# Kernel optimization log

Hardware: AMD Instinct MI355X
Metric: run time of the kernel (lower is better)

## Reference

```python
import jax, jax.numpy as jnp
import numpy as np
import math

B, L, D, P = 2, 2048, 256, 32
PI = math.pi


def _layernorm(x, g, b, eps=1e-5):
    m = x.mean(-1, keepdims=True)
    v = x.var(-1, keepdims=True)
    return (x - m) / jnp.sqrt(v + eps) * g + b


def setup_inputs() -> dict:
    key = jax.random.key(0)
    ks = jax.random.split(key, 16)
    sd = 1.0 / math.sqrt(D)
    f32 = jnp.float32
    inp = {
        "x": jax.random.normal(ks[0], (B, L, D), f32),
        # key_encoder: Linear(D, P)
        "key_W": jax.random.normal(ks[1], (D, P), f32) * sd,
        "key_b": jnp.zeros((P,), f32),
        # value_encoder: Linear(D, D)
        "val_W": jax.random.normal(ks[2], (D, D), f32) * sd,
        "val_b": jnp.zeros((D,), f32),
        # refiner: LayerNorm(D), Linear(D, 2D), GELU, Linear(2D, D)
        "ln1_g": jnp.ones((D,), f32),
        "ln1_b": jnp.zeros((D,), f32),
        "W1": jax.random.normal(ks[3], (D, 2 * D), f32) * sd,
        "b1": jnp.zeros((2 * D,), f32),
        "W2": jax.random.normal(ks[4], (2 * D, D), f32) * (1.0 / math.sqrt(2 * D)),
        "b2": jnp.zeros((D,), f32),
        # to_out: LayerNorm(D), Linear(D, D)
        "ln2_g": jnp.ones((D,), f32),
        "ln2_b": jnp.zeros((D,), f32),
        "Wo": jax.random.normal(ks[5], (D, D), f32) * sd,
        "bo": jnp.zeros((D,), f32),
    }
    return inp


def reference(x, key_W, key_b, val_W, val_b, ln1_g, ln1_b, W1, b1, W2, b2,
              ln2_g, ln2_b, Wo, bo):
    # key phases in (-pi, pi); phasor exp(i*theta) handled as (cos, sin)
    phases = jnp.tanh(x @ key_W + key_b) * PI          # (B, L, P)
    values = x @ val_W + val_b                          # (B, L, D)

    cos_p = jnp.cos(phases)
    sin_p = jnp.sin(phases)
    # torch.roll(shifts=1, dims=1) then zero the first position -> shift right, row 0 = 0
    zrow = jnp.zeros_like(cos_p[:, :1])
    cos_s = jnp.concatenate([zrow, cos_p[:, :-1]], axis=1)
    sin_s = jnp.concatenate([zrow, sin_p[:, :-1]], axis=1)

    # odd positions hold values
    vmask = (jnp.arange(L) % 2 == 1).astype(x.dtype)    # (L,)
    mv = values * vmask[None, :, None]                  # (B, L, D)

    # bind: outer product phasor (P) x value (D); real/imag parts
    bound_re = cos_s[..., None] * mv[:, :, None, :]     # (B, L, P, D)
    bound_im = sin_s[..., None] * mv[:, :, None, :]
    mem_re = jnp.cumsum(bound_re, axis=1)
    mem_im = jnp.cumsum(bound_im, axis=1)

    # retrieve: Re[ memory * exp(-i*theta) ] summed over phases
    retrieved = (jnp.einsum('blpd,blp->bld', mem_re, cos_p)
                 + jnp.einsum('blpd,blp->bld', mem_im, sin_p))

    valid = jnp.maximum(jnp.cumsum(vmask), 1.0)         # (L,)
    retrieved = retrieved / (jnp.sqrt(valid)[None, :, None] * math.sqrt(P))

    h = _layernorm(retrieved, ln1_g, ln1_b)
    h = jax.nn.gelu(h @ W1 + b1, approximate=False)
    refined = h @ W2 + b2
    out = x + (_layernorm(refined, ln2_g, ln2_b) @ Wo + bo)
    return out
```

## Files before the change

### kernel.cpp

```cpp
#include <hip/hip_runtime.h>
#include <math.h>

#define BB 2
#define LL 2048
#define DD 256
#define PP 32
#define NC 64
#define PI_F 3.14159265358979323846f

typedef __attribute__((ext_vector_type(8))) short bf16x8;
typedef __attribute__((ext_vector_type(4))) float f32x4;
typedef unsigned short ushort_t;
typedef unsigned int uint_t;

__device__ inline ushort_t f2bf(float x) {
    uint_t u = __float_as_uint(x);
    uint_t r = (u + 0x7fffu + ((u >> 16) & 1u)) >> 16;
    return (ushort_t)r;
}

__global__ __launch_bounds__(256) void prep_key_kernel(
    const float* __restrict__ W1, const float* __restrict__ W2,
    const float* __restrict__ Wo, const float* __restrict__ valW,
    const float* __restrict__ x, const float* __restrict__ key_W,
    const float* __restrict__ key_b,
    ushort_t* __restrict__ W1t, ushort_t* __restrict__ W2t,
    ushort_t* __restrict__ Wot, ushort_t* __restrict__ valWt,
    float2* __restrict__ ph)
{
    const int bid = blockIdx.x;
    const int t = threadIdx.x;
    if (bid < 96) {
        __shared__ float T[64][65];
        const float* W; ushort_t* Wt; int K, N, tile;
        if (bid < 32)      { W = W1;   Wt = W1t;   K = 256; N = 512; tile = bid; }
        else if (bid < 64) { W = W2;   Wt = W2t;   K = 512; N = 256; tile = bid - 32; }
        else if (bid < 80) { W = Wo;   Wt = Wot;   K = 256; N = 256; tile = bid - 64; }
        else               { W = valW; Wt = valWt; K = 256; N = 256; tile = bid - 80; }
        const int ntiles = N / 64;
        const int k0 = (tile / ntiles) * 64, n0 = (tile % ntiles) * 64;
        {
            const int rr = t >> 2, cb = (t & 3) * 16;
            #pragma unroll
            for (int i = 0; i < 16; i += 4) {
                const float4 v = *(const float4*)&W[(k0 + rr) * N + n0 + cb + i];
                T[rr][cb + i + 0] = v.x; T[rr][cb + i + 1] = v.y;
                T[rr][cb + i + 2] = v.z; T[rr][cb + i + 3] = v.w;
            }
        }
        __syncthreads();
        {
            const int n = t >> 2, kb = (t & 3) * 16;
            #pragma unroll
            for (int i = 0; i < 16; ++i)
                Wt[(n0 + n) * K + k0 + kb + i] = f2bf(T[kb + i][n]);
        }
    } else {
        __shared__ ushort_t xt[16][264];
        __shared__ ushort_t kwT[32][264];
        __shared__ float rbuf[4][2][16][17];
        const int row0 = (bid - 96) * 16;
        {
            const int l = t >> 4, cb = (t & 15) * 16;
            const float* src = &x[(long)(row0 + l) * DD + cb];
            ushort_t tmp[16];
            #pragma unroll
            for (int i = 0; i < 4; ++i) {
                const float4 v = *(const float4*)&src[i * 4];
                tmp[i*4+0] = f2bf(v.x); tmp[i*4+1] = f2bf(v.y);
                tmp[i*4+2] = f2bf(v.z); tmp[i*4+3] = f2bf(v.w);
            }
            *(uint4*)&xt[l][cb]     = *(uint4*)&tmp[0];
            *(uint4*)&xt[l][cb + 8] = *(uint4*)&tmp[8];
        }
        {
            #pragma unroll
            for (int i = 0; i < 8; ++i) {
                const int idx4 = i * 256 + t;
                const int k = idx4 >> 3, pc = (idx4 & 7) * 4;
                const float4 v = *(const float4*)&key_W[k * 32 + pc];
                kwT[pc + 0][k] = f2bf(v.x);
                kwT[pc + 1][k] = f2bf(v.y);
                kwT[pc + 2][k] = f2bf(v.z);
                kwT[pc + 3][k] = f2bf(v.w);
            }
        }
        __syncthreads();
        const int wv = t >> 6, lane = t & 63;
        const int qd = lane >> 4, mc = lane & 15;
        f32x4 acc0 = {0.f,0.f,0.f,0.f}, acc1 = {0.f,0.f,0.f,0.f};
        #pragma unroll
        for (int ks = 0; ks < 2; ++ks) {
            const int ko = wv * 64 + ks * 32 + qd * 8;
            const bf16x8 a  = *(const bf16x8*)&xt[mc][ko];
            const bf16x8 b0 = *(const bf16x8*)&kwT[mc][ko];
            const bf16x8 b1 = *(const bf16x8*)&kwT[16 + mc][ko];
            acc0 = __builtin_amdgcn_mfma_f32_16x16x32_bf16(a, b0, acc0, 0, 0, 0);
            acc1 = __builtin_amdgcn_mfma_f32_16x16x32_bf16(a, b1, acc1, 0, 0, 0);
        }
        #pragma unroll
        for (int r = 0; r < 4; ++r) {
            rbuf[wv][0][qd * 4 + r][mc] = acc0[r];
            rbuf[wv][1][qd * 4 + r][mc] = acc1[r];
        }
        __syncthreads();
        #pragma unroll
        for (int rep = 0; rep < 2; ++rep) {
            const int idx = rep * 256 + t;
            const int p = idx & 31, l = idx >> 5;
            const int nf = p >> 4, mcol = p & 15;
            float a = key_b[p] + rbuf[0][nf][l][mcol] + rbuf[1][nf][l][mcol]
                    + rbuf[2][nf][l][mcol] + rbuf[3][nf][l][mcol];
            a = tanhf(a) * PI_F;
            float sn, cs;
            sincosf(a, &sn, &cs);
            ph[(long)(row0 + l) * PP + p] = make_float2(cs, sn);
        }
    }
}

__global__ __launch_bounds__(256) void valbind_kernel(
    const float* __restrict__ x, const float2* __restrict__ ph,
    const ushort_t* __restrict__ valWt, const float* __restrict__ val_b,
    ushort_t* __restrict__ VoddT, float* __restrict__ Mt)
{
    __shared__ ushort_t xsb[16][264];
    __shared__ ushort_t VdT[64][40];
    __shared__ ushort_t phsT[64][40];
    __shared__ float    Ms[64][68];

    const int tid = threadIdx.x;
    const int bid = blockIdx.x;
    const int b  = bid >> 8;
    const int c  = (bid >> 2) & 63;
    const int dq = bid & 3;
    const int base = b * LL;
    const int r0 = 32 * c;

    {
        const int j = tid >> 4, cb = (tid & 15) * 16;
        const float* src = &x[(long)(base + r0 + 2 * j + 1) * DD + cb];
        ushort_t tmp[16];
        #pragma unroll
        for (int i = 0; i < 4; ++i) {
            const float4 v = *(const float4*)&src[i * 4];
            tmp[i*4+0] = f2bf(v.x); tmp[i*4+1] = f2bf(v.y);
            tmp[i*4+2] = f2bf(v.z); tmp[i*4+3] = f2bf(v.w);
        }
        *(uint4*)&xsb[j][cb]     = *(uint4*)&tmp[0];
        *(uint4*)&xsb[j][cb + 8] = *(uint4*)&tmp[8];
    }
    {
        const int j = tid >> 4, qb = (tid & 15) * 4;
        const float4 v = *(const float4*)((const float*)ph +
                              (long)(base + r0 + 2 * j) * 64 + qb);
        phsT[qb + 0][j] = f2bf(v.x);
        phsT[qb + 1][j] = f2bf(v.y);
        phsT[qb + 2][j] = f2bf(v.z);
        phsT[qb + 3][j] = f2bf(v.w);
    }
    for (int e = tid; e < 64 * 16; e += 256) {
        phsT[e >> 4][16 + (e & 15)] = 0;
        VdT[e >> 4][16 + (e & 15)] = 0;
    }
    __syncthreads();

    const int wv = tid >> 6, lane = tid & 63;
    const int qd = lane >> 4, mc = lane & 15;

    f32x4 va = {0.f,0.f,0.f,0.f};
    const int dloc = wv * 16 + mc;
    const int ng = dq * 64 + dloc;
    const ushort_t* B0 = &valWt[(long)ng * 256];
    #pragma unroll
    for (int ks = 0; ks < 8; ++ks) {
        const bf16x8 a  = *(const bf16x8*)&xsb[mc][ks * 32 + qd * 8];
        const bf16x8 b0 = *(const bf16x8*)&B0[ks * 32 + qd * 8];
        va = __builtin_amdgcn_mfma_f32_16x16x32_bf16(a, b0, va, 0, 0, 0);
    }
    {
        const float bb = val_b[ng];
        #pragma unroll
        for (int r = 0; r < 4; ++r)
            VdT[dloc][qd * 4 + r] = f2bf(va[r] + bb);
    }
    __syncthreads();

    const bf16x8 a2 = *(const bf16x8*)&phsT[wv * 16 + mc][qd * 8];
    f32x4 macc[4];
    #pragma unroll
    for (int nf = 0; nf < 4; ++nf) {
        f32x4 z = {0.f,0.f,0.f,0.f};
        const bf16x8 b2 = *(const bf16x8*)&VdT[nf * 16 + mc][qd * 8];
        macc[nf] = __builtin_amdgcn_mfma_f32_16x16x32_bf16(a2, b2, z, 0, 0, 0);
    }
    #pragma unroll
    for (int nf = 0; nf < 4; ++nf) {
        #pragma unroll
        for (int r = 0; r < 4; ++r)
            Ms[nf * 16 + mc][wv * 16 + qd * 4 + r] = macc[nf][r];
    }
    __syncthreads();

    {
        float* dst = &Mt[((long)(b * NC + c) * 256 + dq * 64) * 64];
        #pragma unroll
        for (int p = 0; p < 4; ++p) {
            const int idx4 = p * 256 + tid;
            const int dl = idx4 >> 4, q4 = (idx4 & 15) * 4;
            *(float4*)&dst[dl * 64 + q4] = *(const float4*)&Ms[dl][q4];
        }
    }
    if (tid < 64) {
        ushort_t* vd = &VoddT[((long)(b * NC + c) * 256 + dq * 64 + tid) * 16];
        *(uint4*)&vd[0] = *(const uint4*)&VdT[tid][0];
        *(uint4*)&vd[8] = *(const uint4*)&VdT[tid][8];
    }
}

__global__ __launch_bounds__(256) void prefix_kernel(
    const float* __restrict__ M, ushort_t* __restrict__ Mpre_b)
{
    __shared__ float segsum[4][64];
    const int tid = threadIdx.x;
    const int b  = blockIdx.x >> 8;
    const int cg = blockIdx.x & 255;
    const int col = cg * 64 + (tid & 63);
    const int seg = tid >> 6;
    const long base = (long)b * NC * 16384 + col;

    float v[16], s = 0.f;
    #pragma unroll
    for (int i = 0; i < 16; ++i) {
        v[i] = M[base + (long)(seg * 16 + i) * 16384];
        s += v[i];
    }
    segsum[seg][tid & 63] = s;
    __syncthreads();
    float run = 0.f;
    #pragma unroll
    for (int sg = 0; sg < 3; ++sg)
        if (sg < seg) run += segsum[sg][tid & 63];
    #pragma unroll
    for (int i = 0; i < 16; ++i) {
        const long a = base + (long)(seg * 16 + i) * 16384;
        Mpre_b[a] = f2bf(run);
        run += v[i];
    }
}

__global__ __launch_bounds__(256) void retrieve_kernel(
    const float* __restrict__ ph, const ushort_t* __restrict__ Mpre_b,
    const ushort_t* __restrict__ VoddT,
    const float* __restrict__ ln1_g, const float* __restrict__ ln1_b,
    ushort_t* __restrict__ rhat)
{
    __shared__ ushort_t Bs_m[256][72];
    __shared__ ushort_t Bs_v[256][32];
    __shared__ ushort_t As_ph[16][72];
    __shared__ ushort_t Bs_sh[16][72];
    __shared__ ushort_t As_p[16][32];
    __shared__ float    ref[16][264];

    const int tid = threadIdx.x;
    const int b = blockIdx.x >> 7;
    const int c = (blockIdx.x >> 1) & 63;
    const int h = blockIdx.x & 1;
    const int l0g = 32 * c + 16 * h;
    const long rowbase = (long)b * LL + l0g;

    {
        const ushort_t* src = &Mpre_b[(long)(b * NC + c) * 16384];
        #pragma unroll
        for (int p = 0; p < 8; ++p) {
            const int idx8 = p * 256 + tid;
            const int d = idx8 >> 3, q8 = (idx8 & 7) * 8;
            *(uint4*)&Bs_m[d][q8] = *(const uint4*)&src[idx8 * 8];
        }
    }
    {
        const int r = tid >> 4, q4 = (tid & 15) * 4;
        const float4 v = *(const float4*)&ph[(rowbase + r) * 64 + q4];
        ushort_t t0[4] = {f2bf(v.x), f2bf(v.y), f2bf(v.z), f2bf(v.w)};
        *(uint2*)&As_ph[r][q4] = *(uint2*)t0;
        const float4 w = *(const float4*)&ph[((long)b * LL + 32 * c + 2 * r) * 64 + q4];
        ushort_t t1[4] = {f2bf(w.x), f2bf(w.y), f2bf(w.z), f2bf(w.w)};
        *(uint2*)&Bs_sh[r][q4] = *(uint2*)t1;
    }
    {
        const ushort_t* src = &VoddT[(long)(b * NC + c) * 4096];
        const int j0 = (tid & 1) * 8;
        *(uint4*)&Bs_v[tid >> 1][j0] = *(const uint4*)&src[tid * 8];
        *(uint4*)&Bs_v[(tid + 256) >> 1][j0] = *(const uint4*)&src[(tid + 256) * 8];
        *(uint4*)&Bs_v[tid][16] = make_uint4(0, 0, 0, 0);
        *(uint4*)&Bs_v[tid][24] = make_uint4(0, 0, 0, 0);
        As_p[tid >> 4][16 + (tid & 15)] = 0;
    }
    __syncthreads();

    const int wv = tid >> 6, lane = tid & 63;
    const int qd = lane >> 4, mc = lane & 15;

    {
        f32x4 sacc = {0.f, 0.f, 0.f, 0.f};
        #pragma unroll
        for (int ks = 0; ks < 2; ++ks) {
            const bf16x8 a  = *(const bf16x8*)&As_ph[mc][ks * 32 + qd * 8];
            const bf16x8 bb = *(const bf16x8*)&Bs_sh[mc][ks * 32 + qd * 8];
            sacc = __builtin_amdgcn_mfma_f32_16x16x32_bf16(a, bb, sacc, 0, 0, 0);
        }
        if (wv == 0) {
            #pragma unroll
            for (int r = 0; r < 4; ++r) {
                const int l = qd * 4 + r;
                As_p[l][mc] = (2 * mc + 1 <= 16 * h + l) ? f2bf(sacc[r])
                                                         : (ushort_t)0;
            }
        }
    }

    f32x4 acc[4];
    #pragma unroll
    for (int i = 0; i < 4; ++i) acc[i] = (f32x4){0.f, 0.f, 0.f, 0.f};
    #pragma unroll
    for (int i = 0; i < 4; ++i) {
        const int d0 = wv * 64 + i * 16;
        #pragma unroll
        for (int ks = 0; ks < 2; ++ks) {
            const bf16x8 a  = *(const bf16x8*)&As_ph[mc][ks * 32 + qd * 8];
            const bf16x8 bb = *(const bf16x8*)&Bs_m[d0 + mc][ks * 32 + qd * 8];
            acc[i] = __builtin_amdgcn_mfma_f32_16x16x32_bf16(a, bb, acc[i], 0, 0, 0);
        }
    }
    __syncthreads();

    {
        const bf16x8 a2 = *(const bf16x8*)&As_p[mc][qd * 8];
        #pragma unroll
        for (int i = 0; i < 4; ++i) {
            const int d0 = wv * 64 + i * 16;
            const bf16x8 b2 = *(const bf16x8*)&Bs_v[d0 + mc][qd * 8];
            acc[i] = __builtin_amdgcn_mfma_f32_16x16x32_bf16(a2, b2, acc[i], 0, 0, 0);
        }
    }

    #pragma unroll
    for (int r = 0; r < 4; ++r) {
        const int l = qd * 4 + r;
        int va = (l0g + l + 1) >> 1; if (va < 1) va = 1;
        const float sc = 0.17677669529663687f * rsqrtf((float)va);
        #pragma unroll
        for (int i = 0; i < 4; ++i)
            ref[l][wv * 64 + i * 16 + mc] = acc[i][r] * sc;
    }
    __syncthreads();

    {
        const int row = tid >> 4, cg = (tid & 15) * 16;
        float s = 0.f, sq = 0.f;
        #pragma unroll
        for (int i = 0; i < 16; ++i) {
            const float v = ref[row][cg + i];
            s += v; sq += v * v;
        }
        s += __shfl_xor(s, 1, 16);  sq += __shfl_xor(sq, 1, 16);
        s += __shfl_xor(s, 2, 16);  sq += __shfl_xor(sq, 2, 16);
        s += __shfl_xor(s, 4, 16);  sq += __shfl_xor(sq, 4, 16);
        s += __shfl_xor(s, 8, 16);  sq += __shfl_xor(sq, 8, 16);
        const float m = s * (1.f / 256.f);
        const float inv = rsqrtf(sq * (1.f / 256.f) - m * m + 1e-5f);
        ushort_t o16[16];
        #pragma unroll
        for (int i = 0; i < 16; ++i) {
            const int cc = cg + i;
            o16[i] = f2bf((ref[row][cc] - m) * inv * ln1_g[cc] + ln1_b[cc]);
        }
        ushort_t* dst = &rhat[(rowbase + row) * DD + cg];
        *(uint4*)&dst[0] = *(uint4*)&o16[0];
        *(uint4*)&dst[8] = *(uint4*)&o16[8];
    }
}

__global__ __launch_bounds__(256) void gemm1_kernel(
    const ushort_t* __restrict__ A, const ushort_t* __restrict__ Bt,
    const float* __restrict__ bias, ushort_t* __restrict__ out)
{
    __shared__ ushort_t As[32][136];
    __shared__ ushort_t Bs[64][136];
    const int tid = threadIdx.x;
    const int mt = blockIdx.x & 127;
    const int nt = blockIdx.x >> 7;
    const int m0 = mt * 32, n0 = nt * 64;
    const int wv = tid >> 6, lane = tid & 63;
    const int qd = lane >> 4, mc = lane & 15;

    f32x4 acc0 = {0.f, 0.f, 0.f, 0.f};
    f32x4 acc1 = {0.f, 0.f, 0.f, 0.f};

    const int ar = tid >> 3, ak = (tid & 7) * 16;
    const int bn = tid >> 2, bk = (tid & 3) * 32;

    for (int k0 = 0; k0 < 256; k0 += 128) {
        __syncthreads();
        {
            const ushort_t* sa = &A[(long)(m0 + ar) * 256 + k0 + ak];
            *(uint4*)&As[ar][ak]     = *(const uint4*)&sa[0];
            *(uint4*)&As[ar][ak + 8] = *(const uint4*)&sa[8];
        }
        {
            const ushort_t* src = &Bt[(long)(n0 + bn) * 256 + k0 + bk];
            *(uint4*)&Bs[bn][bk +  0] = *(const uint4*)&src[0];
            *(uint4*)&Bs[bn][bk +  8] = *(const uint4*)&src[8];
            *(uint4*)&Bs[bn][bk + 16] = *(const uint4*)&src[16];
            *(uint4*)&Bs[bn][bk + 24] = *(const uint4*)&src[24];
        }
        __syncthreads();
        #pragma unroll
        for (int ko = 0; ko < 128; ko += 32) {
            const bf16x8 a0 = *(const bf16x8*)&As[mc][ko + qd * 8];
            const bf16x8 a1 = *(const bf16x8*)&As[16 + mc][ko + qd * 8];
            const bf16x8 b  = *(const bf16x8*)&Bs[wv * 16 + mc][ko + qd * 8];
            acc0 = __builtin_amdgcn_mfma_f32_16x16x32_bf16(a0, b, acc0, 0, 0, 0);
            acc1 = __builtin_amdgcn_mfma_f32_16x16x32_bf16(a1, b, acc1, 0, 0, 0);
        }
    }

    const int nn = n0 + wv * 16 + mc;
    const float bb = bias[nn];
    #pragma unroll
    for (int r = 0; r < 4; ++r) {
        const long row0w = m0 + qd * 4 + r;
        float v0 = acc0[r] + bb;
        float v1 = acc1[r] + bb;
        v0 = 0.5f * v0 * (1.f + erff(v0 * 0.70710678118654752f));
        v1 = 0.5f * v1 * (1.f + erff(v1 * 0.70710678118654752f));
        out[row0w * 512 + nn] = f2bf(v0);
        out[(row0w + 16) * 512 + nn] = f2bf(v1);
    }
}

__global__ __launch_bounds__(256) void gemm23_kernel(
    const ushort_t* __restrict__ h, const ushort_t* __restrict__ W2t,
    const float* __restrict__ b2, const float* __restrict__ ln2_g,
    const float* __restrict__ ln2_b, const ushort_t* __restrict__ Wot,
    const float* __restrict__ bo, const float* __restrict__ x,
    float* __restrict__ out)
{
    __shared__ ushort_t As[16][72];
    __shared__ ushort_t Bs[256][72];
    __shared__ float Ct[16][264];
    __shared__ ushort_t shT[16][264];

    const int tid = threadIdx.x;
    const int m0 = blockIdx.x * 16;
    const int wv = tid >> 6, lane = tid & 63;
    const int qd = lane >> 4, mc = lane & 15;

    f32x4 acc[4];
    #pragma unroll
    for (int nf = 0; nf < 4; ++nf) acc[nf] = (f32x4){0.f,0.f,0.f,0.f};

    const int sr = tid >> 3, sk = (tid & 7) * 8;

    for (int k0 = 0; k0 < 512; k0 += 64) {
        __syncthreads();
        if (tid < 128)
            *(uint4*)&As[sr][sk] = *(const uint4*)&h[(long)(m0 + sr) * 512 + k0 + sk];
        #pragma unroll
        for (int rr = 0; rr < 8; ++rr) {
            const int n = rr * 32 + (tid >> 3);
            *(uint4*)&Bs[n][sk] = *(const uint4*)&W2t[(long)n * 512 + k0 + sk];
        }
        __syncthreads();
        #pragma unroll
        for (int ks = 0; ks < 2; ++ks) {
            const bf16x8 a = *(const bf16x8*)&As[mc][ks * 32 + qd * 8];
            #pragma unroll
            for (int nf = 0; nf < 4; ++nf) {
                const bf16x8 b = *(const bf16x8*)&Bs[wv * 64 + nf * 16 + mc][ks * 32 + qd * 8];
                acc[nf] = __builtin_amdgcn_mfma_f32_16x16x32_bf16(a, b, acc[nf], 0, 0, 0);
            }
        }
    }

    #pragma unroll
    for (int nf = 0; nf < 4; ++nf) {
        const int n = wv * 64 + nf * 16 + mc;
        const float bb = b2[n];
        #pragma unroll
        for (int r = 0; r < 4; ++r)
            Ct[qd * 4 + r][n] = acc[nf][r] + bb;
    }
    __syncthreads();

    {
        const int row = tid >> 4, cg = (tid & 15) * 16;
        float s = 0.f, sq = 0.f;
        #pragma unroll
        for (int i = 0; i < 16; ++i) {
            const float v = Ct[row][cg + i];
            s += v; sq += v * v;
        }
        s  += __shfl_xor(s, 1, 16);  sq += __shfl_xor(sq, 1, 16);
        s  += __shfl_xor(s, 2, 16);  sq += __shfl_xor(sq, 2, 16);
        s  += __shfl_xor(s, 4, 16);  sq += __shfl_xor(sq, 4, 16);
        s  += __shfl_xor(s, 8, 16);  sq += __shfl_xor(sq, 8, 16);
        const float m = s * (1.f / 256.f);
        const float inv = rsqrtf(sq * (1.f / 256.f) - m * m + 1e-5f);
        #pragma unroll
        for (int i = 0; i < 16; ++i) {
            const int cc = cg + i;
            shT[row][cc] = f2bf((Ct[row][cc] - m) * inv * ln2_g[cc] + ln2_b[cc]);
        }
    }

    f32x4 acc2[4];
    #pragma unroll
    for (int nf = 0; nf < 4; ++nf) acc2[nf] = (f32x4){0.f,0.f,0.f,0.f};

    for (int k0 = 0; k0 < 256; k0 += 64) {
        __syncthreads();
        #pragma unroll
        for (int rr = 0; rr < 8; ++rr) {
            const int n = rr * 32 + (tid >> 3);
            *(uint4*)&Bs[n][sk] = *(const uint4*)&Wot[(long)n * 256 + k0 + sk];
        }
        __syncthreads();
        #pragma unroll
        for (int ks = 0; ks < 2; ++ks) {
            const bf16x8 a = *(const bf16x8*)&shT[mc][k0 + ks * 32 + qd * 8];
            #pragma unroll
            for (int nf = 0; nf < 4; ++nf) {
                const bf16x8 b = *(const bf16x8*)&Bs[wv * 64 + nf * 16 + mc][ks * 32 + qd * 8];
                acc2[nf] = __builtin_amdgcn_mfma_f32_16x16x32_bf16(a, b, acc2[nf], 0, 0, 0);
            }
        }
    }

    #pragma unroll
    for (int nf = 0; nf < 4; ++nf) {
        const int n = wv * 64 + nf * 16 + mc;
        const float bb = bo[n];
        #pragma unroll
        for (int r = 0; r < 4; ++r) {
            const long row = m0 + qd * 4 + r;
            out[row * DD + n] = acc2[nf][r] + bb + x[row * DD + n];
        }
    }
}

extern "C" void kernel_launch(void* const* d_in, const int* in_sizes, int n_in,
                              void* d_out, int out_size, void* d_ws, size_t ws_size,
                              hipStream_t stream)
{
    const float* x     = (const float*)d_in[0];
    const float* key_W = (const float*)d_in[1];
    const float* key_b = (const float*)d_in[2];
    const float* val_W = (const float*)d_in[3];
    const float* val_b = (const float*)d_in[4];
    const float* ln1_g = (const float*)d_in[5];
    const float* ln1_b = (const float*)d_in[6];
    const float* W1    = (const float*)d_in[7];
    const float* b1    = (const float*)d_in[8];
    const float* W2    = (const float*)d_in[9];
    const float* b2    = (const float*)d_in[10];
    const float* ln2_g = (const float*)d_in[11];
    const float* ln2_b = (const float*)d_in[12];
    const float* Wo    = (const float*)d_in[13];
    const float* bo    = (const float*)d_in[14];
    float* outp = (float*)d_out;

    float* ws = (float*)d_ws;
    float*  ph      = ws;
    float*  Mt      = ws + 262144;
    ushort_t* Mpre_b = (ushort_t*)(Mt + 2097152);
    ushort_t* VoddT  = Mpre_b + 2097152;
    ushort_t* rhat_b = VoddT + 524288;
    ushort_t* W1t   = rhat_b + 1048576;
    ushort_t* W2t   = W1t + 131072;
    ushort_t* Wot   = W2t + 131072;
    ushort_t* valWt = Wot + 65536;
    ushort_t* h_b    = (ushort_t*)Mt;

    prep_key_kernel<<<352, 256, 0, stream>>>(W1, W2, Wo, val_W, x, key_W, key_b,
                                             W1t, W2t, Wot, valWt, (float2*)ph);
    valbind_kernel<<<512, 256, 0, stream>>>(x, (const float2*)ph, valWt, val_b,
                                            VoddT, Mt);
    prefix_kernel<<<512, 256, 0, stream>>>(Mt, Mpre_b);
    retrieve_kernel<<<256, 256, 0, stream>>>(ph, Mpre_b, VoddT, ln1_g, ln1_b, rhat_b);
    gemm1_kernel<<<1024, 256, 0, stream>>>(rhat_b, W1t, b1, h_b);
    gemm23_kernel<<<256, 256, 0, stream>>>(h_b, W2t, b2, ln2_g, ln2_b,
                                           Wot, bo, x, outp);
}
```

Before: 124.1 us.

## Fuse GEMM1+GELU into the GEMM2/LayerNorm/GEMM3 kernel via shared-memory hidden tile

Merges the first MLP GEMM with GELU into the kernel that performs the second GEMM, LayerNorm and output projection. Each 16-row block computes its 512-wide hidden activation into shared memory instead of writing it to global memory. This removes a kernel launch and the global round trip of the hidden tensor. In exchange each block streams all of W1 serially over 8 tiles, and GEMM1 runs at lower parallelism than the separate 1024-block launch.

```diff
diff --git a/kernel.cpp b/kernel.cpp
--- a/kernel.cpp
+++ b/kernel.cpp
@@ -381,115 +381,90 @@
     }
 }
 
-__global__ __launch_bounds__(256) void gemm1_kernel(
-    const ushort_t* __restrict__ A, const ushort_t* __restrict__ Bt,
-    const float* __restrict__ bias, ushort_t* __restrict__ out)
-{
-    __shared__ ushort_t As[32][136];
-    __shared__ ushort_t Bs[64][136];
-    const int tid = threadIdx.x;
-    const int mt = blockIdx.x & 127;
-    const int nt = blockIdx.x >> 7;
-    const int m0 = mt * 32, n0 = nt * 64;
-    const int wv = tid >> 6, lane = tid & 63;
-    const int qd = lane >> 4, mc = lane & 15;
-
-    f32x4 acc0 = {0.f, 0.f, 0.f, 0.f};
-    f32x4 acc1 = {0.f, 0.f, 0.f, 0.f};
-
-    const int ar = tid >> 3, ak = (tid & 7) * 16;
-    const int bn = tid >> 2, bk = (tid & 3) * 32;
-
-    for (int k0 = 0; k0 < 256; k0 += 128) {
-        __syncthreads();
-        {
-            const ushort_t* sa = &A[(long)(m0 + ar) * 256 + k0 + ak];
-            *(uint4*)&As[ar][ak]     = *(const uint4*)&sa[0];
-            *(uint4*)&As[ar][ak + 8] = *(const uint4*)&sa[8];
-        }
-        {
-            const ushort_t* src = &Bt[(long)(n0 + bn) * 256 + k0 + bk];
-            *(uint4*)&Bs[bn][bk +  0] = *(const uint4*)&src[0];
-            *(uint4*)&Bs[bn][bk +  8] = *(const uint4*)&src[8];
-            *(uint4*)&Bs[bn][bk + 16] = *(const uint4*)&src[16];
-            *(uint4*)&Bs[bn][bk + 24] = *(const uint4*)&src[24];
-        }
-        __syncthreads();
-        #pragma unroll
-        for (int ko = 0; ko < 128; ko += 32) {
-            const bf16x8 a0 = *(const bf16x8*)&As[mc][ko + qd * 8];
-            const bf16x8 a1 = *(const bf16x8*)&As[16 + mc][ko + qd * 8];
-            const bf16x8 b  = *(const bf16x8*)&Bs[wv * 16 + mc][ko + qd * 8];
-            acc0 = __builtin_amdgcn_mfma_f32_16x16x32_bf16(a0, b, acc0, 0, 0, 0);
-            acc1 = __builtin_amdgcn_mfma_f32_16x16x32_bf16(a1, b, acc1, 0, 0, 0);
-        }
-    }
-
-    const int nn = n0 + wv * 16 + mc;
-    const float bb = bias[nn];
-    #pragma unroll
-    for (int r = 0; r < 4; ++r) {
-        const long row0w = m0 + qd * 4 + r;
-        float v0 = acc0[r] + bb;
-        float v1 = acc1[r] + bb;
-        v0 = 0.5f * v0 * (1.f + erff(v0 * 0.70710678118654752f));
-        v1 = 0.5f * v1 * (1.f + erff(v1 * 0.70710678118654752f));
-        out[row0w * 512 + nn] = f2bf(v0);
-        out[(row0w + 16) * 512 + nn] = f2bf(v1);
-    }
-}
-
-__global__ __launch_bounds__(256) void gemm23_kernel(
-    const ushort_t* __restrict__ h, const ushort_t* __restrict__ W2t,
+__global__ __launch_bounds__(256) void mlp_kernel(
+    const ushort_t* __restrict__ rhat, const ushort_t* __restrict__ W1t,
+    const float* __restrict__ b1, const ushort_t* __restrict__ W2t,
     const float* __restrict__ b2, const float* __restrict__ ln2_g,
     const float* __restrict__ ln2_b, const ushort_t* __restrict__ Wot,
     const float* __restrict__ bo, const float* __restrict__ x,
     float* __restrict__ out)
 {
-    __shared__ ushort_t As[16][72];
-    __shared__ ushort_t Bs[256][72];
-    __shared__ float Ct[16][264];
-    __shared__ ushort_t shT[16][264];
+    __shared__ ushort_t AsR[16][264];
+    __shared__ ushort_t Bpool[256 * 72];
+    __shared__ ushort_t hT[16][520];
 
     const int tid = threadIdx.x;
     const int m0 = blockIdx.x * 16;
     const int wv = tid >> 6, lane = tid & 63;
     const int qd = lane >> 4, mc = lane & 15;
 
-    f32x4 acc[4];
-    #pragma unroll
-    for (int nf = 0; nf < 4; ++nf) acc[nf] = (f32x4){0.f,0.f,0.f,0.f};
-
-    const int sr = tid >> 3, sk = (tid & 7) * 8;
-
+    {
+        const int r = tid >> 4, cb = (tid & 15) * 16;
+        const ushort_t* src = &rhat[(long)(m0 + r) * DD + cb];
+        *(uint4*)&AsR[r][cb]     = *(const uint4*)&src[0];
+        *(uint4*)&AsR[r][cb + 8] = *(const uint4*)&src[8];
+    }
+
+    for (int nt = 0; nt < 8; ++nt) {
+        const int n0 = nt * 64;
+        __syncthreads();
+        {
+            const int row = tid >> 2, kc = (tid & 3) * 64;
+            const ushort_t* src = &W1t[(long)(n0 + row) * 256 + kc];
+            ushort_t* dst = &Bpool[row * 264 + kc];
+            #pragma unroll
+            for (int i = 0; i < 8; ++i)
+                *(uint4*)&dst[i * 8] = *(const uint4*)&src[i * 8];
+        }
+        __syncthreads();
+        f32x4 acc = {0.f, 0.f, 0.f, 0.f};
+        #pragma unroll
+        for (int ks = 0; ks < 8; ++ks) {
+            const bf16x8 a = *(const bf16x8*)&AsR[mc][ks * 32 + qd * 8];
+            const bf16x8 b = *(const bf16x8*)&Bpool[(wv * 16 + mc) * 264 + ks * 32 + qd * 8];
+            acc = __builtin_amdgcn_mfma_f32_16x16x32_bf16(a, b, acc, 0, 0, 0);
+        }
+        const int nn = n0 + wv * 16 + mc;
+        const float bb = b1[nn];
+        #pragma unroll
+        for (int r = 0; r < 4; ++r) {
+            float v = acc[r] + bb;
+            v = 0.5f * v * (1.f + erff(v * 0.70710678118654752f));
+            hT[qd * 4 + r][nn] = f2bf(v);
+        }
+    }
+
+    f32x4 acc2[4];
+    #pragma unroll
+    for (int nf = 0; nf < 4; ++nf) acc2[nf] = (f32x4){0.f,0.f,0.f,0.f};
+    const int sk = (tid & 7) * 8;
     for (int k0 = 0; k0 < 512; k0 += 64) {
         __syncthreads();
-        if (tid < 128)
-            *(uint4*)&As[sr][sk] = *(const uint4*)&h[(long)(m0 + sr) * 512 + k0 + sk];
         #pragma unroll
         for (int rr = 0; rr < 8; ++rr) {
             const int n = rr * 32 + (tid >> 3);
-            *(uint4*)&Bs[n][sk] = *(const uint4*)&W2t[(long)n * 512 + k0 + sk];
+            *(uint4*)&Bpool[n * 72 + sk] = *(const uint4*)&W2t[(long)n * 512 + k0 + sk];
         }
         __syncthreads();
         #pragma unroll
         for (int ks = 0; ks < 2; ++ks) {
-            const bf16x8 a = *(const bf16x8*)&As[mc][ks * 32 + qd * 8];
+            const bf16x8 a = *(const bf16x8*)&hT[mc][k0 + ks * 32 + qd * 8];
             #pragma unroll
             for (int nf = 0; nf < 4; ++nf) {
-                const bf16x8 b = *(const bf16x8*)&Bs[wv * 64 + nf * 16 + mc][ks * 32 + qd * 8];
-                acc[nf] = __builtin_amdgcn_mfma_f32_16x16x32_bf16(a, b, acc[nf], 0, 0, 0);
+                const bf16x8 b = *(const bf16x8*)&Bpool[(wv * 64 + nf * 16 + mc) * 72 + ks * 32 + qd * 8];
+                acc2[nf] = __builtin_amdgcn_mfma_f32_16x16x32_bf16(a, b, acc2[nf], 0, 0, 0);
             }
         }
     }
-
+    __syncthreads();
+    float* Ctf = (float*)Bpool;
     #pragma unroll
     for (int nf = 0; nf < 4; ++nf) {
         const int n = wv * 64 + nf * 16 + mc;
         const float bb = b2[n];
         #pragma unroll
         for (int r = 0; r < 4; ++r)
-            Ct[qd * 4 + r][n] = acc[nf][r] + bb;
+            Ctf[(qd * 4 + r) * 264 + n] = acc2[nf][r] + bb;
     }
     __syncthreads();
 
@@ -498,7 +473,7 @@
         float s = 0.f, sq = 0.f;
         #pragma unroll
         for (int i = 0; i < 16; ++i) {
-            const float v = Ct[row][cg + i];
+            const float v = Ctf[row * 264 + cg + i];
             s += v; sq += v * v;
         }
         s  += __shfl_xor(s, 1, 16);  sq += __shfl_xor(sq, 1, 16);
@@ -510,29 +485,28 @@
         #pragma unroll
         for (int i = 0; i < 16; ++i) {
             const int cc = cg + i;
-            shT[row][cc] = f2bf((Ct[row][cc] - m) * inv * ln2_g[cc] + ln2_b[cc]);
-        }
-    }
-
-    f32x4 acc2[4];
-    #pragma unroll
-    for (int nf = 0; nf < 4; ++nf) acc2[nf] = (f32x4){0.f,0.f,0.f,0.f};
-
+            AsR[row][cc] = f2bf((Ctf[row * 264 + cc] - m) * inv * ln2_g[cc] + ln2_b[cc]);
+        }
+    }
+
+    f32x4 acc3[4];
+    #pragma unroll
+    for (int nf = 0; nf < 4; ++nf) acc3[nf] = (f32x4){0.f,0.f,0.f,0.f};
     for (int k0 = 0; k0 < 256; k0 += 64) {
         __syncthreads();
         #pragma unroll
         for (int rr = 0; rr < 8; ++rr) {
             const int n = rr * 32 + (tid >> 3);
-            *(uint4*)&Bs[n][sk] = *(const uint4*)&Wot[(long)n * 256 + k0 + sk];
+            *(uint4*)&Bpool[n * 72 + sk] = *(const uint4*)&Wot[(long)n * 256 + k0 + sk];
         }
         __syncthreads();
         #pragma unroll
         for (int ks = 0; ks < 2; ++ks) {
-            const bf16x8 a = *(const bf16x8*)&shT[mc][k0 + ks * 32 + qd * 8];
+            const bf16x8 a = *(const bf16x8*)&AsR[mc][k0 + ks * 32 + qd * 8];
             #pragma unroll
             for (int nf = 0; nf < 4; ++nf) {
-                const bf16x8 b = *(const bf16x8*)&Bs[wv * 64 + nf * 16 + mc][ks * 32 + qd * 8];
-                acc2[nf] = __builtin_amdgcn_mfma_f32_16x16x32_bf16(a, b, acc2[nf], 0, 0, 0);
+                const bf16x8 b = *(const bf16x8*)&Bpool[(wv * 64 + nf * 16 + mc) * 72 + ks * 32 + qd * 8];
+                acc3[nf] = __builtin_amdgcn_mfma_f32_16x16x32_bf16(a, b, acc3[nf], 0, 0, 0);
             }
         }
     }
@@ -544,7 +518,7 @@
         #pragma unroll
         for (int r = 0; r < 4; ++r) {
             const long row = m0 + qd * 4 + r;
-            out[row * DD + n] = acc2[nf][r] + bb + x[row * DD + n];
+            out[row * DD + n] = acc3[nf][r] + bb + x[row * DD + n];
         }
     }
 }
@@ -580,7 +554,6 @@
     ushort_t* W2t   = W1t + 131072;
     ushort_t* Wot   = W2t + 131072;
     ushort_t* valWt = Wot + 65536;
-    ushort_t* h_b    = (ushort_t*)Mt;
 
     prep_key_kernel<<<352, 256, 0, stream>>>(W1, W2, Wo, val_W, x, key_W, key_b,
                                              W1t, W2t, Wot, valWt, (float2*)ph);
@@ -588,7 +561,6 @@
                                             VoddT, Mt);
     prefix_kernel<<<512, 256, 0, stream>>>(Mt, Mpre_b);
     retrieve_kernel<<<256, 256, 0, stream>>>(ph, Mpre_b, VoddT, ln1_g, ln1_b, rhat_b);
-    gemm1_kernel<<<1024, 256, 0, stream>>>(rhat_b, W1t, b1, h_b);
-    gemm23_kernel<<<256, 256, 0, stream>>>(h_b, W2t, b2, ln2_g, ln2_b,
-                                           Wot, bo, x, outp);
-}
+    mlp_kernel<<<256, 256, 0, stream>>>(rhat_b, W1t, b1, W2t, b2, ln2_g, ln2_b,
+                                        Wot, bo, x, outp);
+}
```

After: 132.2 us. +6.5%, slower.

## Fuse valbind, prefix and retrieve into one cooperative kernel with grid syncs

Applied to the files above, without the earlier changes.

Merges the three middle kernels (value projection and bind, chunk prefix scan, retrieve with layernorm) into a single cooperative launch of 512 blocks. Grid-wide syncs replace the kernel boundaries, and the three phases share one statically sized shared-memory buffer. The aim is to remove two launch gaps and their drain and refill time. In exchange it pays grid-sync cost, leaves half the blocks idle in the retrieve phase, and needs all 512 blocks co-resident; the large shared-memory allocation may limit occupancy.

```diff
diff --git a/kernel.cpp b/kernel.cpp
--- a/kernel.cpp
+++ b/kernel.cpp
@@ -1,5 +1,8 @@
 #include <hip/hip_runtime.h>
+#include <hip/hip_cooperative_groups.h>
 #include <math.h>
+
+namespace cg = cooperative_groups;
 
 #define BB 2
 #define LL 2048
@@ -119,265 +122,263 @@
     }
 }
 
-__global__ __launch_bounds__(256) void valbind_kernel(
-    const float* __restrict__ x, const float2* __restrict__ ph,
+__global__ __launch_bounds__(256, 2) void middle_kernel(
+    const float* __restrict__ x, const float* __restrict__ ph,
     const ushort_t* __restrict__ valWt, const float* __restrict__ val_b,
-    ushort_t* __restrict__ VoddT, float* __restrict__ Mt)
-{
-    __shared__ ushort_t xsb[16][264];
-    __shared__ ushort_t VdT[64][40];
-    __shared__ ushort_t phsT[64][40];
-    __shared__ float    Ms[64][68];
-
-    const int tid = threadIdx.x;
-    const int bid = blockIdx.x;
-    const int b  = bid >> 8;
-    const int c  = (bid >> 2) & 63;
-    const int dq = bid & 3;
-    const int base = b * LL;
-    const int r0 = 32 * c;
-
-    {
-        const int j = tid >> 4, cb = (tid & 15) * 16;
-        const float* src = &x[(long)(base + r0 + 2 * j + 1) * DD + cb];
-        ushort_t tmp[16];
-        #pragma unroll
-        for (int i = 0; i < 4; ++i) {
-            const float4 v = *(const float4*)&src[i * 4];
-            tmp[i*4+0] = f2bf(v.x); tmp[i*4+1] = f2bf(v.y);
-            tmp[i*4+2] = f2bf(v.z); tmp[i*4+3] = f2bf(v.w);
-        }
-        *(uint4*)&xsb[j][cb]     = *(uint4*)&tmp[0];
-        *(uint4*)&xsb[j][cb + 8] = *(uint4*)&tmp[8];
-    }
-    {
-        const int j = tid >> 4, qb = (tid & 15) * 4;
-        const float4 v = *(const float4*)((const float*)ph +
-                              (long)(base + r0 + 2 * j) * 64 + qb);
-        phsT[qb + 0][j] = f2bf(v.x);
-        phsT[qb + 1][j] = f2bf(v.y);
-        phsT[qb + 2][j] = f2bf(v.z);
-        phsT[qb + 3][j] = f2bf(v.w);
-    }
-    for (int e = tid; e < 64 * 16; e += 256) {
-        phsT[e >> 4][16 + (e & 15)] = 0;
-        VdT[e >> 4][16 + (e & 15)] = 0;
-    }
-    __syncthreads();
-
-    const int wv = tid >> 6, lane = tid & 63;
-    const int qd = lane >> 4, mc = lane & 15;
-
-    f32x4 va = {0.f,0.f,0.f,0.f};
-    const int dloc = wv * 16 + mc;
-    const int ng = dq * 64 + dloc;
-    const ushort_t* B0 = &valWt[(long)ng * 256];
-    #pragma unroll
-    for (int ks = 0; ks < 8; ++ks) {
-        const bf16x8 a  = *(const bf16x8*)&xsb[mc][ks * 32 + qd * 8];
-        const bf16x8 b0 = *(const bf16x8*)&B0[ks * 32 + qd * 8];
-        va = __builtin_amdgcn_mfma_f32_16x16x32_bf16(a, b0, va, 0, 0, 0);
-    }
-    {
-        const float bb = val_b[ng];
-        #pragma unroll
-        for (int r = 0; r < 4; ++r)
-            VdT[dloc][qd * 4 + r] = f2bf(va[r] + bb);
-    }
-    __syncthreads();
-
-    const bf16x8 a2 = *(const bf16x8*)&phsT[wv * 16 + mc][qd * 8];
-    f32x4 macc[4];
-    #pragma unroll
-    for (int nf = 0; nf < 4; ++nf) {
-        f32x4 z = {0.f,0.f,0.f,0.f};
-        const bf16x8 b2 = *(const bf16x8*)&VdT[nf * 16 + mc][qd * 8];
-        macc[nf] = __builtin_amdgcn_mfma_f32_16x16x32_bf16(a2, b2, z, 0, 0, 0);
-    }
-    #pragma unroll
-    for (int nf = 0; nf < 4; ++nf) {
-        #pragma unroll
-        for (int r = 0; r < 4; ++r)
-            Ms[nf * 16 + mc][wv * 16 + qd * 4 + r] = macc[nf][r];
-    }
-    __syncthreads();
-
-    {
-        float* dst = &Mt[((long)(b * NC + c) * 256 + dq * 64) * 64];
-        #pragma unroll
-        for (int p = 0; p < 4; ++p) {
-            const int idx4 = p * 256 + tid;
-            const int dl = idx4 >> 4, q4 = (idx4 & 15) * 4;
-            *(float4*)&dst[dl * 64 + q4] = *(const float4*)&Ms[dl][q4];
-        }
-    }
-    if (tid < 64) {
-        ushort_t* vd = &VoddT[((long)(b * NC + c) * 256 + dq * 64 + tid) * 16];
-        *(uint4*)&vd[0] = *(const uint4*)&VdT[tid][0];
-        *(uint4*)&vd[8] = *(const uint4*)&VdT[tid][8];
-    }
-}
-
-__global__ __launch_bounds__(256) void prefix_kernel(
-    const float* __restrict__ M, ushort_t* __restrict__ Mpre_b)
-{
-    __shared__ float segsum[4][64];
-    const int tid = threadIdx.x;
-    const int b  = blockIdx.x >> 8;
-    const int cg = blockIdx.x & 255;
-    const int col = cg * 64 + (tid & 63);
-    const int seg = tid >> 6;
-    const long base = (long)b * NC * 16384 + col;
-
-    float v[16], s = 0.f;
-    #pragma unroll
-    for (int i = 0; i < 16; ++i) {
-        v[i] = M[base + (long)(seg * 16 + i) * 16384];
-        s += v[i];
-    }
-    segsum[seg][tid & 63] = s;
-    __syncthreads();
-    float run = 0.f;
-    #pragma unroll
-    for (int sg = 0; sg < 3; ++sg)
-        if (sg < seg) run += segsum[sg][tid & 63];
-    #pragma unroll
-    for (int i = 0; i < 16; ++i) {
-        const long a = base + (long)(seg * 16 + i) * 16384;
-        Mpre_b[a] = f2bf(run);
-        run += v[i];
-    }
-}
-
-__global__ __launch_bounds__(256) void retrieve_kernel(
-    const float* __restrict__ ph, const ushort_t* __restrict__ Mpre_b,
-    const ushort_t* __restrict__ VoddT,
+    ushort_t* __restrict__ VoddT, float* __restrict__ Mt,
+    ushort_t* __restrict__ Mpre_b,
     const float* __restrict__ ln1_g, const float* __restrict__ ln1_b,
     ushort_t* __restrict__ rhat)
 {
-    __shared__ ushort_t Bs_m[256][72];
-    __shared__ ushort_t Bs_v[256][32];
-    __shared__ ushort_t As_ph[16][72];
-    __shared__ ushort_t Bs_sh[16][72];
-    __shared__ ushort_t As_p[16][32];
-    __shared__ float    ref[16][264];
-
+    __shared__ __align__(16) char smem[75776];
+    cg::grid_group grid = cg::this_grid();
     const int tid = threadIdx.x;
-    const int b = blockIdx.x >> 7;
-    const int c = (blockIdx.x >> 1) & 63;
-    const int h = blockIdx.x & 1;
-    const int l0g = 32 * c + 16 * h;
-    const long rowbase = (long)b * LL + l0g;
-
-    {
-        const ushort_t* src = &Mpre_b[(long)(b * NC + c) * 16384];
-        #pragma unroll
-        for (int p = 0; p < 8; ++p) {
-            const int idx8 = p * 256 + tid;
-            const int d = idx8 >> 3, q8 = (idx8 & 7) * 8;
-            *(uint4*)&Bs_m[d][q8] = *(const uint4*)&src[idx8 * 8];
-        }
-    }
-    {
-        const int r = tid >> 4, q4 = (tid & 15) * 4;
-        const float4 v = *(const float4*)&ph[(rowbase + r) * 64 + q4];
-        ushort_t t0[4] = {f2bf(v.x), f2bf(v.y), f2bf(v.z), f2bf(v.w)};
-        *(uint2*)&As_ph[r][q4] = *(uint2*)t0;
-        const float4 w = *(const float4*)&ph[((long)b * LL + 32 * c + 2 * r) * 64 + q4];
-        ushort_t t1[4] = {f2bf(w.x), f2bf(w.y), f2bf(w.z), f2bf(w.w)};
-        *(uint2*)&Bs_sh[r][q4] = *(uint2*)t1;
-    }
-    {
-        const ushort_t* src = &VoddT[(long)(b * NC + c) * 4096];
-        const int j0 = (tid & 1) * 8;
-        *(uint4*)&Bs_v[tid >> 1][j0] = *(const uint4*)&src[tid * 8];
-        *(uint4*)&Bs_v[(tid + 256) >> 1][j0] = *(const uint4*)&src[(tid + 256) * 8];
-        *(uint4*)&Bs_v[tid][16] = make_uint4(0, 0, 0, 0);
-        *(uint4*)&Bs_v[tid][24] = make_uint4(0, 0, 0, 0);
-        As_p[tid >> 4][16 + (tid & 15)] = 0;
-    }
-    __syncthreads();
-
+    const int bid = blockIdx.x;
     const int wv = tid >> 6, lane = tid & 63;
     const int qd = lane >> 4, mc = lane & 15;
 
     {
-        f32x4 sacc = {0.f, 0.f, 0.f, 0.f};
-        #pragma unroll
-        for (int ks = 0; ks < 2; ++ks) {
-            const bf16x8 a  = *(const bf16x8*)&As_ph[mc][ks * 32 + qd * 8];
-            const bf16x8 bb = *(const bf16x8*)&Bs_sh[mc][ks * 32 + qd * 8];
-            sacc = __builtin_amdgcn_mfma_f32_16x16x32_bf16(a, bb, sacc, 0, 0, 0);
-        }
-        if (wv == 0) {
-            #pragma unroll
-            for (int r = 0; r < 4; ++r) {
-                const int l = qd * 4 + r;
-                As_p[l][mc] = (2 * mc + 1 <= 16 * h + l) ? f2bf(sacc[r])
-                                                         : (ushort_t)0;
-            }
-        }
-    }
-
-    f32x4 acc[4];
-    #pragma unroll
-    for (int i = 0; i < 4; ++i) acc[i] = (f32x4){0.f, 0.f, 0.f, 0.f};
-    #pragma unroll
-    for (int i = 0; i < 4; ++i) {
-        const int d0 = wv * 64 + i * 16;
-        #pragma unroll
-        for (int ks = 0; ks < 2; ++ks) {
-            const bf16x8 a  = *(const bf16x8*)&As_ph[mc][ks * 32 + qd * 8];
-            const bf16x8 bb = *(const bf16x8*)&Bs_m[d0 + mc][ks * 32 + qd * 8];
-            acc[i] = __builtin_amdgcn_mfma_f32_16x16x32_bf16(a, bb, acc[i], 0, 0, 0);
-        }
-    }
-    __syncthreads();
+        ushort_t (*xsb)[264] = (ushort_t(*)[264])(smem);
+        ushort_t (*VdT)[40]  = (ushort_t(*)[40])(smem + 8448);
+        ushort_t (*phsT)[40] = (ushort_t(*)[40])(smem + 13568);
+        float    (*Ms)[68]   = (float(*)[68])(smem + 18688);
+
+        const int b  = bid >> 8;
+        const int c  = (bid >> 2) & 63;
+        const int dq = bid & 3;
+        const int base = b * LL;
+        const int r0 = 32 * c;
+
+        {
+            const int j = tid >> 4, cb = (tid & 15) * 16;
+            const float* src = &x[(long)(base + r0 + 2 * j + 1) * DD + cb];
+            ushort_t tmp[16];
+            #pragma unroll
+            for (int i = 0; i < 4; ++i) {
+                const float4 v = *(const float4*)&src[i * 4];
+                tmp[i*4+0] = f2bf(v.x); tmp[i*4+1] = f2bf(v.y);
+                tmp[i*4+2] = f2bf(v.z); tmp[i*4+3] = f2bf(v.w);
+            }
+            *(uint4*)&xsb[j][cb]     = *(uint4*)&tmp[0];
+            *(uint4*)&xsb[j][cb + 8] = *(uint4*)&tmp[8];
+        }
+        {
+            const int j = tid >> 4, qb = (tid & 15) * 4;
+            const float4 v = *(const float4*)&ph[(long)(base + r0 + 2 * j) * 64 + qb];
+            phsT[qb + 0][j] = f2bf(v.x);
+            phsT[qb + 1][j] = f2bf(v.y);
+            phsT[qb + 2][j] = f2bf(v.z);
+            phsT[qb + 3][j] = f2bf(v.w);
+        }
+        for (int e = tid; e < 64 * 16; e += 256) {
+            phsT[e >> 4][16 + (e & 15)] = 0;
+            VdT[e >> 4][16 + (e & 15)] = 0;
+        }
+        __syncthreads();
+
+        f32x4 va = {0.f,0.f,0.f,0.f};
+        const int dloc = wv * 16 + mc;
+        const int ng = dq * 64 + dloc;
+        const ushort_t* B0 = &valWt[(long)ng * 256];
+        #pragma unroll
+        for (int ks = 0; ks < 8; ++ks) {
+            const bf16x8 a  = *(const bf16x8*)&xsb[mc][ks * 32 + qd * 8];
+            const bf16x8 b0 = *(const bf16x8*)&B0[ks * 32 + qd * 8];
+            va = __builtin_amdgcn_mfma_f32_16x16x32_bf16(a, b0, va, 0, 0, 0);
+        }
+        {
+            const float bb = val_b[ng];
+            #pragma unroll
+            for (int r = 0; r < 4; ++r)
+                VdT[dloc][qd * 4 + r] = f2bf(va[r] + bb);
+        }
+        __syncthreads();
+
+        const bf16x8 a2 = *(const bf16x8*)&phsT[wv * 16 + mc][qd * 8];
+        f32x4 macc[4];
+        #pragma unroll
+        for (int nf = 0; nf < 4; ++nf) {
+            f32x4 z = {0.f,0.f,0.f,0.f};
+            const bf16x8 b2 = *(const bf16x8*)&VdT[nf * 16 + mc][qd * 8];
+            macc[nf] = __builtin_amdgcn_mfma_f32_16x16x32_bf16(a2, b2, z, 0, 0, 0);
+        }
+        #pragma unroll
+        for (int nf = 0; nf < 4; ++nf) {
+            #pragma unroll
+            for (int r = 0; r < 4; ++r)
+                Ms[nf * 16 + mc][wv * 16 + qd * 4 + r] = macc[nf][r];
+        }
+        __syncthreads();
+
+        {
+            float* dst = &Mt[((long)(b * NC + c) * 256 + dq * 64) * 64];
+            #pragma unroll
+            for (int p = 0; p < 4; ++p) {
+                const int idx4 = p * 256 + tid;
+                const int dl = idx4 >> 4, q4 = (idx4 & 15) * 4;
+                *(float4*)&dst[dl * 64 + q4] = *(const float4*)&Ms[dl][q4];
+            }
+        }
+        if (tid < 64) {
+            ushort_t* vd = &VoddT[((long)(b * NC + c) * 256 + dq * 64 + tid) * 16];
+            *(uint4*)&vd[0] = *(const uint4*)&VdT[tid][0];
+            *(uint4*)&vd[8] = *(const uint4*)&VdT[tid][8];
+        }
+    }
+    __threadfence();
+    grid.sync();
 
     {
-        const bf16x8 a2 = *(const bf16x8*)&As_p[mc][qd * 8];
+        float (*segsum)[64] = (float(*)[64])(smem);
+        const int b  = bid >> 8;
+        const int cg2 = bid & 255;
+        const int col = cg2 * 64 + (tid & 63);
+        const int seg = tid >> 6;
+        const long base = (long)b * NC * 16384 + col;
+
+        float v[16], s = 0.f;
+        #pragma unroll
+        for (int i = 0; i < 16; ++i) {
+            v[i] = Mt[base + (long)(seg * 16 + i) * 16384];
+            s += v[i];
+        }
+        segsum[seg][tid & 63] = s;
+        __syncthreads();
+        float run = 0.f;
+        #pragma unroll
+        for (int sg = 0; sg < 3; ++sg)
+            if (sg < seg) run += segsum[sg][tid & 63];
+        #pragma unroll
+        for (int i = 0; i < 16; ++i) {
+            const long a = base + (long)(seg * 16 + i) * 16384;
+            Mpre_b[a] = f2bf(run);
+            run += v[i];
+        }
+    }
+    __threadfence();
+    grid.sync();
+
+    if (bid < 256) {
+        ushort_t (*Bs_m)[72]  = (ushort_t(*)[72])(smem);
+        ushort_t (*Bs_v)[32]  = (ushort_t(*)[32])(smem + 36864);
+        ushort_t (*As_ph)[72] = (ushort_t(*)[72])(smem + 53248);
+        ushort_t (*Bs_sh)[72] = (ushort_t(*)[72])(smem + 55552);
+        ushort_t (*As_p)[32]  = (ushort_t(*)[32])(smem + 57856);
+        float    (*ref)[264]  = (float(*)[264])(smem + 58880);
+
+        const int b = bid >> 7;
+        const int c = (bid >> 1) & 63;
+        const int h = bid & 1;
+        const int l0g = 32 * c + 16 * h;
+        const long rowbase = (long)b * LL + l0g;
+
+        {
+            const ushort_t* src = &Mpre_b[(long)(b * NC + c) * 16384];
+            #pragma unroll
+            for (int p = 0; p < 8; ++p) {
+                const int idx8 = p * 256 + tid;
+                const int d = idx8 >> 3, q8 = (idx8 & 7) * 8;
+                *(uint4*)&Bs_m[d][q8] = *(const uint4*)&src[idx8 * 8];
+            }
+        }
+        {
+            const int r = tid >> 4, q4 = (tid & 15) * 4;
+            const float4 v = *(const float4*)&ph[(rowbase + r) * 64 + q4];
+            ushort_t t0[4] = {f2bf(v.x), f2bf(v.y), f2bf(v.z), f2bf(v.w)};
+            *(uint2*)&As_ph[r][q4] = *(uint2*)t0;
+            const float4 w = *(const float4*)&ph[((long)b * LL + 32 * c + 2 * r) * 64 + q4];
+            ushort_t t1[4] = {f2bf(w.x), f2bf(w.y), f2bf(w.z), f2bf(w.w)};
+            *(uint2*)&Bs_sh[r][q4] = *(uint2*)t1;
+        }
+        {
+            const ushort_t* src = &VoddT[(long)(b * NC + c) * 4096];
+            const int j0 = (tid & 1) * 8;
+            *(uint4*)&Bs_v[tid >> 1][j0] = *(const uint4*)&src[tid * 8];
+            *(uint4*)&Bs_v[(tid + 256) >> 1][j0] = *(const uint4*)&src[(tid + 256) * 8];
+            *(uint4*)&Bs_v[tid][16] = make_uint4(0, 0, 0, 0);
+            *(uint4*)&Bs_v[tid][24] = make_uint4(0, 0, 0, 0);
+            As_p[tid >> 4][16 + (tid & 15)] = 0;
+        }
+        __syncthreads();
+
+        {
+            f32x4 sacc = {0.f, 0.f, 0.f, 0.f};
+            #pragma unroll
+            for (int ks = 0; ks < 2; ++ks) {
+                const bf16x8 a  = *(const bf16x8*)&As_ph[mc][ks * 32 + qd * 8];
+                const bf16x8 bb = *(const bf16x8*)&Bs_sh[mc][ks * 32 + qd * 8];
+                sacc = __builtin_amdgcn_mfma_f32_16x16x32_bf16(a, bb, sacc, 0, 0, 0);
+            }
+            if (wv == 0) {
+                #pragma unroll
+                for (int r = 0; r < 4; ++r) {
+                    const int l = qd * 4 + r;
+                    As_p[l][mc] = (2 * mc + 1 <= 16 * h + l) ? f2bf(sacc[r])
+                                                             : (ushort_t)0;
+                }
+            }
+        }
+
+        f32x4 acc[4];
+        #pragma unroll
+        for (int i = 0; i < 4; ++i) acc[i] = (f32x4){0.f, 0.f, 0.f, 0.f};
         #pragma unroll
         for (int i = 0; i < 4; ++i) {
             const int d0 = wv * 64 + i * 16;
-            const bf16x8 b2 = *(const bf16x8*)&Bs_v[d0 + mc][qd * 8];
-            acc[i] = __builtin_amdgcn_mfma_f32_16x16x32_bf16(a2, b2, acc[i], 0, 0, 0);
-        }
-    }
-
-    #pragma unroll
-    for (int r = 0; r < 4; ++r) {
-        const int l = qd * 4 + r;
-        int va = (l0g + l + 1) >> 1; if (va < 1) va = 1;
-        const float sc = 0.17677669529663687f * rsqrtf((float)va);
-        #pragma unroll
-        for (int i = 0; i < 4; ++i)
-            ref[l][wv * 64 + i * 16 + mc] = acc[i][r] * sc;
-    }
-    __syncthreads();
-
-    {
-        const int row = tid >> 4, cg = (tid & 15) * 16;
-        float s = 0.f, sq = 0.f;
-        #pragma unroll
-        for (int i = 0; i < 16; ++i) {
-            const float v = ref[row][cg + i];
-            s += v; sq += v * v;
-        }
-        s += __shfl_xor(s, 1, 16);  sq += __shfl_xor(sq, 1, 16);
-        s += __shfl_xor(s, 2, 16);  sq += __shfl_xor(sq, 2, 16);
-        s += __shfl_xor(s, 4, 16);  sq += __shfl_xor(sq, 4, 16);
-        s += __shfl_xor(s, 8, 16);  sq += __shfl_xor(sq, 8, 16);
-        const float m = s * (1.f / 256.f);
-        const float inv = rsqrtf(sq * (1.f / 256.f) - m * m + 1e-5f);
-        ushort_t o16[16];
-        #pragma unroll
-        for (int i = 0; i < 16; ++i) {
-            const int cc = cg + i;
-            o16[i] = f2bf((ref[row][cc] - m) * inv * ln1_g[cc] + ln1_b[cc]);
-        }
-        ushort_t* dst = &rhat[(rowbase + row) * DD + cg];
-        *(uint4*)&dst[0] = *(uint4*)&o16[0];
-        *(uint4*)&dst[8] = *(uint4*)&o16[8];
+            #pragma unroll
+            for (int ks = 0; ks < 2; ++ks) {
+                const bf16x8 a  = *(const bf16x8*)&As_ph[mc][ks * 32 + qd * 8];
+                const bf16x8 bb = *(const bf16x8*)&Bs_m[d0 + mc][ks * 32 + qd * 8];
+                acc[i] = __builtin_amdgcn_mfma_f32_16x16x32_bf16(a, bb, acc[i], 0, 0, 0);
+            }
+        }
+        __syncthreads();
+
+        {
+            const bf16x8 a2 = *(const bf16x8*)&As_p[mc][qd * 8];
+            #pragma unroll
+            for (int i = 0; i < 4; ++i) {
+                const int d0 = wv * 64 + i * 16;
+                const bf16x8 b2 = *(const bf16x8*)&Bs_v[d0 + mc][qd * 8];
+                acc[i] = __builtin_amdgcn_mfma_f32_16x16x32_bf16(a2, b2, acc[i], 0, 0, 0);
+            }
+        }
+
+        #pragma unroll
+        for (int r = 0; r < 4; ++r) {
+            const int l = qd * 4 + r;
+            int va = (l0g + l + 1) >> 1; if (va < 1) va = 1;
+            const float sc = 0.17677669529663687f * rsqrtf((float)va);
+            #pragma unroll
+            for (int i = 0; i < 4; ++i)
+                ref[l][wv * 64 + i * 16 + mc] = acc[i][r] * sc;
+        }
+        __syncthreads();
+
+        {
+            const int row = tid >> 4, cg2 = (tid & 15) * 16;
+            float s = 0.f, sq = 0.f;
+            #pragma unroll
+            for (int i = 0; i < 16; ++i) {
+                const float v = ref[row][cg2 + i];
+                s += v; sq += v * v;
+            }
+            s += __shfl_xor(s, 1, 16);  sq += __shfl_xor(sq, 1, 16);
+            s += __shfl_xor(s, 2, 16);  sq += __shfl_xor(sq, 2, 16);
+            s += __shfl_xor(s, 4, 16);  sq += __shfl_xor(sq, 4, 16);
+            s += __shfl_xor(s, 8, 16);  sq += __shfl_xor(sq, 8, 16);
+            const float m = s * (1.f / 256.f);
+            const float inv = rsqrtf(sq * (1.f / 256.f) - m * m + 1e-5f);
+            ushort_t o16[16];
+            #pragma unroll
+            for (int i = 0; i < 16; ++i) {
+                const int cc = cg2 + i;
+                o16[i] = f2bf((ref[row][cc] - m) * inv * ln1_g[cc] + ln1_b[cc]);
+            }
+            ushort_t* dst = &rhat[(rowbase + row) * DD + cg2];
+            *(uint4*)&dst[0] = *(uint4*)&o16[0];
+            *(uint4*)&dst[8] = *(uint4*)&o16[8];
+        }
     }
 }
 
@@ -494,11 +495,11 @@
     __syncthreads();
 
     {
-        const int row = tid >> 4, cg = (tid & 15) * 16;
+        const int row = tid >> 4, cg2 = (tid & 15) * 16;
         float s = 0.f, sq = 0.f;
         #pragma unroll
         for (int i = 0; i < 16; ++i) {
-            const float v = Ct[row][cg + i];
+            const float v = Ct[row][cg2 + i];
             s += v; sq += v * v;
         }
         s  += __shfl_xor(s, 1, 16);  sq += __shfl_xor(sq, 1, 16);
@@ -509,7 +510,7 @@
         const float inv = rsqrtf(sq * (1.f / 256.f) - m * m + 1e-5f);
         #pragma unroll
         for (int i = 0; i < 16; ++i) {
-            const int cc = cg + i;
+            const int cc = cg2 + i;
             shT[row][cc] = f2bf((Ct[row][cc] - m) * inv * ln2_g[cc] + ln2_b[cc]);
         }
     }
@@ -571,23 +572,26 @@
     float* outp = (float*)d_out;
 
     float* ws = (float*)d_ws;
-    float*  ph      = ws;
-    float*  Mt      = ws + 262144;
+    float*  ph       = ws;
+    float*  Mt       = ws + 262144;
     ushort_t* Mpre_b = (ushort_t*)(Mt + 2097152);
     ushort_t* VoddT  = Mpre_b + 2097152;
     ushort_t* rhat_b = VoddT + 524288;
-    ushort_t* W1t   = rhat_b + 1048576;
-    ushort_t* W2t   = W1t + 131072;
-    ushort_t* Wot   = W2t + 131072;
-    ushort_t* valWt = Wot + 65536;
+    ushort_t* W1t    = rhat_b + 1048576;
+    ushort_t* W2t    = W1t + 131072;
+    ushort_t* Wot    = W2t + 131072;
+    ushort_t* valWt  = Wot + 65536;
     ushort_t* h_b    = (ushort_t*)Mt;
 
     prep_key_kernel<<<352, 256, 0, stream>>>(W1, W2, Wo, val_W, x, key_W, key_b,
                                              W1t, W2t, Wot, valWt, (float2*)ph);
-    valbind_kernel<<<512, 256, 0, stream>>>(x, (const float2*)ph, valWt, val_b,
-                                            VoddT, Mt);
-    prefix_kernel<<<512, 256, 0, stream>>>(Mt, Mpre_b);
-    retrieve_kernel<<<256, 256, 0, stream>>>(ph, Mpre_b, VoddT, ln1_g, ln1_b, rhat_b);
+    {
+        void* cargs[] = {(void*)&x, (void*)&ph, (void*)&valWt, (void*)&val_b,
+                         (void*)&VoddT, (void*)&Mt, (void*)&Mpre_b,
+                         (void*)&ln1_g, (void*)&ln1_b, (void*)&rhat_b};
+        hipLaunchCooperativeKernel((void*)middle_kernel, dim3(512), dim3(256),
+                                   cargs, 0, stream);
+    }
     gemm1_kernel<<<1024, 256, 0, stream>>>(rhat_b, W1t, b1, h_b);
     gemm23_kernel<<<256, 256, 0, stream>>>(h_b, W2t, b2, ln2_g, ln2_b,
                                            Wot, bo, x, outp);
```

Measured after the change: 338.7 us. +172.9%, slower.
